# Kernel optimization log

Hardware: AMD Instinct MI355X
Metric: run time of the kernel (lower is better)

The kernel has to match this reference:

```python
import jax, jax.numpy as jnp
import numpy as np

B, S, E, H = 2, 2048, 2048, 16
HD = E // H  # head_dim = 128


def setup_inputs() -> dict:
    key = jax.random.key(0)
    ks = jax.random.split(key, 7)
    inp = {
        "query": jax.random.normal(ks[0], (B, S, E), dtype=jnp.float32),
        "key": jax.random.normal(ks[1], (B, S, E), dtype=jnp.float32),
        "value": jax.random.normal(ks[2], (B, S, E), dtype=jnp.float32),
        # qkv: Linear(E, 3E) -> weight [3E, E], bias [3E]
        "Wqkv": jax.random.normal(ks[3], (3 * E, E), dtype=jnp.float32) * (E ** -0.5),
        "bqkv": jnp.zeros((3 * E,), dtype=jnp.float32),
        # proj: Linear(E, E) (source bug-fixed; see notes)
        "Wproj": jax.random.normal(ks[4], (E, E), dtype=jnp.float32) * (E ** -0.5),
        "bproj": jnp.zeros((E,), dtype=jnp.float32),
    }
    return inp


def reference(query, key, value, Wqkv, bqkv, Wproj, bproj):
    # NB: `key` and `value` are unused by the original forward.
    b, s, _ = query.shape
    qkv = query @ Wqkv.T + bqkv                      # [B, S, 3E]
    qkv = qkv.reshape(b, s, H, 3 * HD).transpose(0, 2, 1, 3)  # [B, H, S, 3*HD]
    q = qkv[..., :HD]
    k = qkv[..., HD:2 * HD]
    v = qkv[..., 2 * HD:]
    # Source divides by scale_factor = HD**-0.5, i.e. MULTIPLIES by sqrt(HD).
    scores = jnp.einsum("bhqd,bhkd->bhqk", q, k) * (HD ** 0.5)
    attn = jax.nn.softmax(scores, axis=-1)           # dropout p=0 -> identity
    out = jnp.einsum("bhqk,bhkd->bhqd", attn, v)     # [B, H, S, HD]
    out = out.transpose(0, 2, 1, 3).reshape(b, s, E)  # [B, S, E]
    return out @ Wproj.T + bproj
```

## Files before the change

### kernel.cpp

```cpp
#include <hip/hip_runtime.h>

#define B_  2
#define S_  2048
#define E_  2048
#define H_  16
#define HD_ 128
#define M_  (B_*S_)
#define N1_ (3*E_)
#define K_  E_

typedef _Float16 f16;
typedef __attribute__((ext_vector_type(8))) _Float16 f16x8;
typedef __attribute__((ext_vector_type(4))) _Float16 f16x4;
typedef __attribute__((ext_vector_type(4))) float    f32x4;
typedef __attribute__((ext_vector_type(4))) float    fv4;

__device__ __forceinline__ void async16(const f16* g, f16* l) {
    __builtin_amdgcn_global_load_lds(
        (const __attribute__((address_space(1))) unsigned int*)g,
        (__attribute__((address_space(3))) unsigned int*)l, 16, 0, 0);
}

__device__ __forceinline__ int swz8(int row, int g) {
    return row * 64 + ((g ^ (row & 7)) << 3);
}
__device__ __forceinline__ int swz16(int row, int g) {
    return row * 128 + ((g ^ (row & 15)) << 3);
}

__device__ __forceinline__ void stage_swz8(const f16* __restrict__ src, int ldg,
                                           f16* lds, int w, int lane) {
#pragma unroll
    for (int i = 0; i < 4; ++i) {
        int p = (w * 4 + i) * 64 + lane;
        int row = p >> 3, gl = p & 7;
        int gs = gl ^ (row & 7);
        async16(src + (size_t)row * ldg + gs * 8, lds + (size_t)p * 8);
    }
}

__device__ __forceinline__ void stage_swz16(const f16* __restrict__ src, int ldg,
                                            f16* lds, int w, int lane) {
#pragma unroll
    for (int i = 0; i < 8; ++i) {
        int p = (w * 8 + i) * 64 + lane;
        int row = p >> 4, gl = p & 15;
        int gs = gl ^ (row & 15);
        async16(src + (size_t)row * ldg + gs * 8, lds + (size_t)p * 8);
    }
}

__device__ __forceinline__ void split8(fv4 a0, fv4 a1, float scale, f16x8& hi, f16x8& lo) {
    float x[8] = {a0.x, a0.y, a0.z, a0.w, a1.x, a1.y, a1.z, a1.w};
#pragma unroll
    for (int e = 0; e < 8; ++e) {
        float xs = x[e] * scale;
        f16 h = (f16)xs;
        hi[e] = h;
        lo[e] = (f16)(xs - (float)h);
    }
}

__global__ void split_f32(const float* __restrict__ src, f16* __restrict__ hi,
                          f16* __restrict__ lo, float scale, int n8) {
    int i = blockIdx.x * blockDim.x + threadIdx.x;
    if (i < n8) {
        fv4 a0 = ((const fv4*)src)[2 * i];
        fv4 a1 = ((const fv4*)src)[2 * i + 1];
        f16x8 h, l;
        split8(a0, a1, scale, h, l);
        ((f16x8*)hi)[i] = h;
        ((f16x8*)lo)[i] = l;
    }
}

__global__ void cvt_f32_f16(const float* __restrict__ src, f16* __restrict__ dst, int n4) {
    int i = blockIdx.x * blockDim.x + threadIdx.x;
    if (i < n4) {
        fv4 v = ((const fv4*)src)[i];
        f16x4 h;
        h.x = (f16)v.x; h.y = (f16)v.y; h.z = (f16)v.z; h.w = (f16)v.w;
        ((f16x4*)dst)[i] = h;
    }
}

template <bool AsyncA>
__global__ __launch_bounds__(256) void gemm_qkv(
    const float* __restrict__ A, const f16* __restrict__ A_hi, const f16* __restrict__ A_lo,
    const f16* __restrict__ W_hi, const f16* __restrict__ W_lo, const float* __restrict__ bias,
    f16* __restrict__ qh, f16* __restrict__ kh, f16* __restrict__ vT)
{
    __shared__ f16 As_hi[128 * 64];
    __shared__ f16 As_lo[128 * 64];
    __shared__ f16 Bs_hi[128 * 64];
    __shared__ f16 Bs_lo[128 * 64];
    const int t = threadIdx.x;
    const int w = t >> 6, lane = t & 63, quad = lane >> 4, l15 = lane & 15;
    const int m0 = blockIdx.y * 128, n0 = blockIdx.x * 128;
    const int wm = (w & 1) * 64, wn = (w >> 1) * 64;
    const int tile_part = (n0 % 384) >> 7;
    const bool need_lo = (tile_part != 2);

    f32x4 acc[4][4];
#pragma unroll
    for (int i = 0; i < 4; ++i)
#pragma unroll
        for (int j = 0; j < 4; ++j) { acc[i][j].x = 0.f; acc[i][j].y = 0.f; acc[i][j].z = 0.f; acc[i][j].w = 0.f; }

    for (int kb = 0; kb < K_ / 64; ++kb) {
        stage_swz8(W_hi + (size_t)n0 * K_ + kb * 64, K_, Bs_hi, w, lane);
        if (need_lo)
            stage_swz8(W_lo + (size_t)n0 * K_ + kb * 64, K_, Bs_lo, w, lane);
        if (AsyncA) {
            stage_swz8(A_hi + (size_t)m0 * K_ + kb * 64, K_, As_hi, w, lane);
            if (need_lo)
                stage_swz8(A_lo + (size_t)m0 * K_ + kb * 64, K_, As_lo, w, lane);
        } else {
            const float* Ag = A + (size_t)m0 * K_ + kb * 64;
#pragma unroll
            for (int i = 0; i < 4; ++i) {
                int gid = t + i * 256;
                int row = gid >> 3, g = gid & 7;
                const float* ap = Ag + (size_t)row * K_ + g * 8;
                fv4 a0 = *(const fv4*)ap;
                fv4 a1 = *(const fv4*)(ap + 4);
                f16x8 hi, lo;
                split8(a0, a1, 1.0f, hi, lo);
                *(f16x8*)&As_hi[swz8(row, g)] = hi;
                *(f16x8*)&As_lo[swz8(row, g)] = lo;
            }
        }
        __syncthreads();

#pragma unroll
        for (int ks = 0; ks < 2; ++ks) {
            f16x8 ah[4], al[4], bh[4], bl[4];
            int g = ks * 4 + quad;
#pragma unroll
            for (int mt = 0; mt < 4; ++mt) {
                int row = wm + mt * 16 + l15;
                ah[mt] = *(const f16x8*)&As_hi[swz8(row, g)];
                al[mt] = *(const f16x8*)&As_lo[swz8(row, g)];
            }
#pragma unroll
            for (int nt = 0; nt < 4; ++nt) {
                int row = wn + nt * 16 + l15;
                bh[nt] = *(const f16x8*)&Bs_hi[swz8(row, g)];
                bl[nt] = *(const f16x8*)&Bs_lo[swz8(row, g)];
            }
#pragma unroll
            for (int mt = 0; mt < 4; ++mt)
#pragma unroll
                for (int nt = 0; nt < 4; ++nt) {
                    acc[mt][nt] = __builtin_amdgcn_mfma_f32_16x16x32_f16(ah[mt], bh[nt], acc[mt][nt], 0, 0, 0);
                    if (need_lo) {
                        acc[mt][nt] = __builtin_amdgcn_mfma_f32_16x16x32_f16(ah[mt], bl[nt], acc[mt][nt], 0, 0, 0);
                        acc[mt][nt] = __builtin_amdgcn_mfma_f32_16x16x32_f16(al[mt], bh[nt], acc[mt][nt], 0, 0, 0);
                    }
                }
        }
        __syncthreads();
    }

    const float inv_s = 1.0f / 64.0f;
#pragma unroll
    for (int nt = 0; nt < 4; ++nt) {
        int n = n0 + wn + nt * 16 + l15;
        float bs = bias[n];
        int h = n / 384;
        int r = n % 384;
        int part = r >> 7;
        int d = r & 127;
#pragma unroll
        for (int mt = 0; mt < 4; ++mt) {
            int mbase = m0 + wm + mt * 16 + quad * 4;
            int b = mbase >> 11, s = mbase & 2047;
            int bh = b * H_ + h;
            if (part == 2) {
                f16x4 pv;
                pv.x = (f16)(acc[mt][nt].x * inv_s + bs);
                pv.y = (f16)(acc[mt][nt].y * inv_s + bs);
                pv.z = (f16)(acc[mt][nt].z * inv_s + bs);
                pv.w = (f16)(acc[mt][nt].w * inv_s + bs);
                *(f16x4*)&vT[((size_t)bh * 128 + d) * 2048 + s] = pv;
            } else {
                f16* dst = (part == 0) ? qh : kh;
                size_t base = (size_t)bh * 2048 * 128;
#pragma unroll
                for (int reg = 0; reg < 4; ++reg)
                    dst[base + (size_t)(s + reg) * 128 + d] = (f16)(acc[mt][nt][reg] * inv_s + bs);
            }
        }
    }
}

__global__ __launch_bounds__(256) void attn(
    const f16* __restrict__ qh, const f16* __restrict__ kh, const f16* __restrict__ vT,
    f16* __restrict__ ao)
{
    __shared__ f16 Ks[128 * 128];
    __shared__ f16 Vts[128 * 128];
    const int t = threadIdx.x;
    const int w = t >> 6, lane = t & 63, quad = lane >> 4, l15 = lane & 15;
    const int bh = blockIdx.y;
    const int q0 = blockIdx.x * 128;
    const f16* Q  = qh + (size_t)bh * 2048 * 128;
    const f16* Kp = kh + (size_t)bh * 2048 * 128;
    const f16* Vp = vT + (size_t)bh * 128 * 2048;

    const float C2 = (float)(11.313708498984761 * 1.4426950408889634);

    f16x8 qf[2][4];
#pragma unroll
    for (int mt = 0; mt < 2; ++mt)
#pragma unroll
        for (int ks = 0; ks < 4; ++ks) {
            int row = q0 + w * 32 + mt * 16 + l15;
            qf[mt][ks] = *(const f16x8*)&Q[(size_t)row * 128 + ks * 32 + quad * 8];
        }

    f32x4 o[2][8];
    float mrow[2][4], lrow[2][4];
#pragma unroll
    for (int mt = 0; mt < 2; ++mt) {
#pragma unroll
        for (int dt = 0; dt < 8; ++dt) { o[mt][dt].x = 0.f; o[mt][dt].y = 0.f; o[mt][dt].z = 0.f; o[mt][dt].w = 0.f; }
#pragma unroll
        for (int reg = 0; reg < 4; ++reg) { mrow[mt][reg] = -1e30f; lrow[mt][reg] = 0.f; }
    }

    for (int j = 0; j < 16; ++j) {
        __syncthreads();
        stage_swz16(Kp + (size_t)(j * 128) * 128, 128, Ks, w, lane);
        stage_swz16(Vp + j * 128, 2048, Vts, w, lane);
        __syncthreads();

        f32x4 sa[2][8];
#pragma unroll
        for (int mt = 0; mt < 2; ++mt)
#pragma unroll
            for (int nt = 0; nt < 8; ++nt) { sa[mt][nt].x = 0.f; sa[mt][nt].y = 0.f; sa[mt][nt].z = 0.f; sa[mt][nt].w = 0.f; }
#pragma unroll
        for (int ks = 0; ks < 4; ++ks) {
            int g = ks * 4 + quad;
            f16x8 bf[8];
#pragma unroll
            for (int nt = 0; nt < 8; ++nt) { int row = nt * 16 + l15; bf[nt] = *(const f16x8*)&Ks[swz16(row, g)]; }
#pragma unroll
            for (int mt = 0; mt < 2; ++mt)
#pragma unroll
                for (int nt = 0; nt < 8; ++nt)
                    sa[mt][nt] = __builtin_amdgcn_mfma_f32_16x16x32_f16(qf[mt][ks], bf[nt], sa[mt][nt], 0, 0, 0);
        }

        float mnew[2][4], alpha[2][4];
#pragma unroll
        for (int mt = 0; mt < 2; ++mt)
#pragma unroll
            for (int reg = 0; reg < 4; ++reg) {
                float mx = sa[mt][0][reg];
#pragma unroll
                for (int nt = 1; nt < 8; ++nt) mx = fmaxf(mx, sa[mt][nt][reg]);
                mx *= C2;
#pragma unroll
                for (int d = 1; d < 16; d <<= 1) mx = fmaxf(mx, __shfl_xor(mx, d));
                float mn = fmaxf(mrow[mt][reg], mx);
                mnew[mt][reg]  = mn;
                alpha[mt][reg] = exp2f(mrow[mt][reg] - mn);
                mrow[mt][reg]  = mn;
            }
#pragma unroll
        for (int mt = 0; mt < 2; ++mt)
#pragma unroll
            for (int reg = 0; reg < 4; ++reg) {
                float rs = 0.f;
#pragma unroll
                for (int nt = 0; nt < 8; ++nt) {
                    float p = exp2f(sa[mt][nt][reg] * C2 - mnew[mt][reg]);
                    sa[mt][nt][reg] = p;
                    rs += p;
                }
#pragma unroll
                for (int d = 1; d < 16; d <<= 1) rs += __shfl_xor(rs, d);
                lrow[mt][reg] = lrow[mt][reg] * alpha[mt][reg] + rs;
#pragma unroll
                for (int dt = 0; dt < 8; ++dt) o[mt][dt][reg] *= alpha[mt][reg];
            }

        __syncthreads();
#pragma unroll
        for (int mt = 0; mt < 2; ++mt)
#pragma unroll
            for (int nt = 0; nt < 8; ++nt) {
                int col = nt * 16 + l15;
#pragma unroll
                for (int reg = 0; reg < 4; ++reg) {
                    int row = w * 32 + mt * 16 + quad * 4 + reg;
                    Ks[row * 128 + (((col >> 3) ^ (row & 15)) << 3) + (col & 7)] = (f16)sa[mt][nt][reg];
                }
            }
        __syncthreads();

#pragma unroll
        for (int ks = 0; ks < 4; ++ks) {
            int g = ks * 4 + quad;
            f16x8 pf[2], vf[8];
#pragma unroll
            for (int mt = 0; mt < 2; ++mt) { int row = w * 32 + mt * 16 + l15; pf[mt] = *(const f16x8*)&Ks[swz16(row, g)]; }
#pragma unroll
            for (int dt = 0; dt < 8; ++dt) { int row = dt * 16 + l15; vf[dt] = *(const f16x8*)&Vts[swz16(row, g)]; }
#pragma unroll
            for (int mt = 0; mt < 2; ++mt)
#pragma unroll
                for (int dt = 0; dt < 8; ++dt)
                    o[mt][dt] = __builtin_amdgcn_mfma_f32_16x16x32_f16(pf[mt], vf[dt], o[mt][dt], 0, 0, 0);
        }
    }

    const int b = bh >> 4, h = bh & 15;
#pragma unroll
    for (int mt = 0; mt < 2; ++mt) {
        float inv[4];
#pragma unroll
        for (int reg = 0; reg < 4; ++reg) inv[reg] = 1.0f / lrow[mt][reg];
#pragma unroll
        for (int dt = 0; dt < 8; ++dt) {
            int col = h * 128 + dt * 16 + l15;
#pragma unroll
            for (int reg = 0; reg < 4; ++reg) {
                int srow = q0 + w * 32 + mt * 16 + quad * 4 + reg;
                ao[(size_t)((b << 11) + srow) * 2048 + col] = (f16)(o[mt][dt][reg] * inv[reg]);
            }
        }
    }
}

__global__ __launch_bounds__(256) void gemm_proj(
    const f16* __restrict__ A, const f16* __restrict__ W, const float* __restrict__ bias,
    float* __restrict__ out)
{
    __shared__ f16 As[128 * 64];
    __shared__ f16 Bs[128 * 64];
    const int t = threadIdx.x;
    const int w = t >> 6, lane = t & 63, quad = lane >> 4, l15 = lane & 15;
    const int m0 = blockIdx.y * 128, n0 = blockIdx.x * 128;
    const int wm = (w & 1) * 64, wn = (w >> 1) * 64;

    f32x4 acc[4][4];
#pragma unroll
    for (int i = 0; i < 4; ++i)
#pragma unroll
        for (int j = 0; j < 4; ++j) { acc[i][j].x = 0.f; acc[i][j].y = 0.f; acc[i][j].z = 0.f; acc[i][j].w = 0.f; }

    for (int kb = 0; kb < K_ / 64; ++kb) {
        stage_swz8(A + (size_t)m0 * K_ + kb * 64, K_, As, w, lane);
        stage_swz8(W + (size_t)n0 * K_ + kb * 64, K_, Bs, w, lane);
        __syncthreads();
#pragma unroll
        for (int ks = 0; ks < 2; ++ks) {
            f16x8 af[4], bf[4];
            int g = ks * 4 + quad;
#pragma unroll
            for (int mt = 0; mt < 4; ++mt) { int row = wm + mt * 16 + l15; af[mt] = *(const f16x8*)&As[swz8(row, g)]; }
#pragma unroll
            for (int nt = 0; nt < 4; ++nt) { int row = wn + nt * 16 + l15; bf[nt] = *(const f16x8*)&Bs[swz8(row, g)]; }
#pragma unroll
            for (int mt = 0; mt < 4; ++mt)
#pragma unroll
                for (int nt = 0; nt < 4; ++nt)
                    acc[mt][nt] = __builtin_amdgcn_mfma_f32_16x16x32_f16(af[mt], bf[nt], acc[mt][nt], 0, 0, 0);
        }
        __syncthreads();
    }

#pragma unroll
    for (int nt = 0; nt < 4; ++nt) {
        int n = n0 + wn + nt * 16 + l15;
        float bs = bias[n];
#pragma unroll
        for (int mt = 0; mt < 4; ++mt) {
            int mbase = m0 + wm + mt * 16 + quad * 4;
#pragma unroll
            for (int reg = 0; reg < 4; ++reg)
                out[(size_t)(mbase + reg) * 2048 + n] = acc[mt][nt][reg] + bs;
        }
    }
}

extern "C" void kernel_launch(void* const* d_in, const int* in_sizes, int n_in,
                              void* d_out, int out_size, void* d_ws, size_t ws_size,
                              hipStream_t stream) {
    const float* query = (const float*)d_in[0];
    const float* Wqkv  = (const float*)d_in[3];
    const float* bqkv  = (const float*)d_in[4];
    const float* Wproj = (const float*)d_in[5];
    const float* bproj = (const float*)d_in[6];
    float* out = (float*)d_out;

    char* ws = (char*)d_ws;
    const size_t MB = 1024ull * 1024ull;
    const bool big = (ws_size >= 128 * MB);

    f16 *A_hi, *A_lo, *W_hi, *W_lo, *qh, *kh, *vT, *ao, *w2;
    if (big) {
        A_hi = (f16*)(ws);
        A_lo = (f16*)(ws + 16 * MB);
        W_hi = (f16*)(ws + 32 * MB);
        W_lo = (f16*)(ws + 56 * MB);
        qh   = (f16*)(ws + 80 * MB);
        kh   = (f16*)(ws + 96 * MB);
        vT   = (f16*)(ws + 112 * MB);
        ao   = (f16*)(ws);
        w2   = (f16*)(ws + 56 * MB);
    } else {
        if (ws_size < 96 * MB) return;
        A_hi = A_lo = nullptr;
        W_hi = (f16*)(ws);
        W_lo = (f16*)(ws + 24 * MB);
        qh   = (f16*)(ws + 48 * MB);
        kh   = (f16*)(ws + 64 * MB);
        vT   = (f16*)(ws + 80 * MB);
        ao   = (f16*)(ws);
        w2   = (f16*)(ws + 24 * MB);
    }

    if (big)
        split_f32<<<(M_ * K_ / 8 + 255) / 256, 256, 0, stream>>>(query, A_hi, A_lo, 1.0f, M_ * K_ / 8);
    split_f32<<<(N1_ * K_ / 8 + 255) / 256, 256, 0, stream>>>(Wqkv, W_hi, W_lo, 64.0f, N1_ * K_ / 8);

    if (big)
        gemm_qkv<true><<<dim3(N1_ / 128, M_ / 128), 256, 0, stream>>>(query, A_hi, A_lo, W_hi, W_lo, bqkv, qh, kh, vT);
    else
        gemm_qkv<false><<<dim3(N1_ / 128, M_ / 128), 256, 0, stream>>>(query, A_hi, A_lo, W_hi, W_lo, bqkv, qh, kh, vT);

    cvt_f32_f16<<<(E_ * E_ / 4 + 255) / 256, 256, 0, stream>>>(Wproj, w2, E_ * E_ / 4);

    attn<<<dim3(S_ / 128, B_ * H_), 256, 0, stream>>>(qh, kh, vT, ao);
    gemm_proj<<<dim3(E_ / 128, M_ / 128), 256, 0, stream>>>(ao, w2, bproj, out);
}
```

Before: 639.5 us.

## Double-buffer 64-key K/V tiles in attention and use private P scratch

The attention kernel now processes 64-key tiles instead of 128 and double-buffers K and V in LDS. The next tile's async loads are issued right after the single top-of-loop barrier, so they overlap with the current tile's QK^T, softmax and PV work. P now goes to a separate per-wave LDS region (Ps) rather than overwriting the K tile, which removes two of the three barriers per iteration. In exchange, LDS use grows from 64KB to 80KB and there are twice as many online-softmax rescale steps, since each tile is smaller.

```diff
diff --git a/kernel.cpp b/kernel.cpp
--- a/kernel.cpp
+++ b/kernel.cpp
@@ -39,14 +39,22 @@
     }
 }
 
-__device__ __forceinline__ void stage_swz16(const f16* __restrict__ src, int ldg,
-                                            f16* lds, int w, int lane) {
-#pragma unroll
-    for (int i = 0; i < 8; ++i) {
-        int p = (w * 8 + i) * 64 + lane;
+__device__ __forceinline__ void stage_k64(const f16* __restrict__ src, f16* lds, int t) {
+#pragma unroll
+    for (int i = 0; i < 4; ++i) {
+        int p = i * 256 + t;
         int row = p >> 4, gl = p & 15;
         int gs = gl ^ (row & 15);
-        async16(src + (size_t)row * ldg + gs * 8, lds + (size_t)p * 8);
+        async16(src + (size_t)row * 128 + gs * 8, lds + (size_t)p * 8);
+    }
+}
+__device__ __forceinline__ void stage_v64(const f16* __restrict__ src, f16* lds, int t) {
+#pragma unroll
+    for (int i = 0; i < 4; ++i) {
+        int p = i * 256 + t;
+        int row = p >> 3, gl = p & 7;
+        int gs = gl ^ (row & 7);
+        async16(src + (size_t)row * 2048 + gs * 8, lds + (size_t)p * 8);
     }
 }
 
@@ -198,8 +206,9 @@
     const f16* __restrict__ qh, const f16* __restrict__ kh, const f16* __restrict__ vT,
     f16* __restrict__ ao)
 {
-    __shared__ f16 Ks[128 * 128];
-    __shared__ f16 Vts[128 * 128];
+    __shared__ f16 Kb[2][64 * 128];
+    __shared__ f16 Vb[2][128 * 64];
+    __shared__ f16 Ps[128 * 64];
     const int t = threadIdx.x;
     const int w = t >> 6, lane = t & 63, quad = lane >> 4, l15 = lane & 15;
     const int bh = blockIdx.y;
@@ -229,27 +238,32 @@
         for (int reg = 0; reg < 4; ++reg) { mrow[mt][reg] = -1e30f; lrow[mt][reg] = 0.f; }
     }
 
-    for (int j = 0; j < 16; ++j) {
+    stage_k64(Kp, Kb[0], t);
+    stage_v64(Vp, Vb[0], t);
+
+    for (int j = 0; j < 32; ++j) {
         __syncthreads();
-        stage_swz16(Kp + (size_t)(j * 128) * 128, 128, Ks, w, lane);
-        stage_swz16(Vp + j * 128, 2048, Vts, w, lane);
-        __syncthreads();
-
-        f32x4 sa[2][8];
+        const int cur = j & 1;
+        if (j < 31) {
+            stage_k64(Kp + (size_t)(j + 1) * 64 * 128, Kb[cur ^ 1], t);
+            stage_v64(Vp + (j + 1) * 64, Vb[cur ^ 1], t);
+        }
+
+        f32x4 sa[2][4];
 #pragma unroll
         for (int mt = 0; mt < 2; ++mt)
 #pragma unroll
-            for (int nt = 0; nt < 8; ++nt) { sa[mt][nt].x = 0.f; sa[mt][nt].y = 0.f; sa[mt][nt].z = 0.f; sa[mt][nt].w = 0.f; }
+            for (int nt = 0; nt < 4; ++nt) { sa[mt][nt].x = 0.f; sa[mt][nt].y = 0.f; sa[mt][nt].z = 0.f; sa[mt][nt].w = 0.f; }
 #pragma unroll
         for (int ks = 0; ks < 4; ++ks) {
             int g = ks * 4 + quad;
-            f16x8 bf[8];
-#pragma unroll
-            for (int nt = 0; nt < 8; ++nt) { int row = nt * 16 + l15; bf[nt] = *(const f16x8*)&Ks[swz16(row, g)]; }
+            f16x8 bf[4];
+#pragma unroll
+            for (int nt = 0; nt < 4; ++nt) { int row = nt * 16 + l15; bf[nt] = *(const f16x8*)&Kb[cur][swz16(row, g)]; }
 #pragma unroll
             for (int mt = 0; mt < 2; ++mt)
 #pragma unroll
-                for (int nt = 0; nt < 8; ++nt)
+                for (int nt = 0; nt < 4; ++nt)
                     sa[mt][nt] = __builtin_amdgcn_mfma_f32_16x16x32_f16(qf[mt][ks], bf[nt], sa[mt][nt], 0, 0, 0);
         }
 
@@ -260,7 +274,7 @@
             for (int reg = 0; reg < 4; ++reg) {
                 float mx = sa[mt][0][reg];
 #pragma unroll
-                for (int nt = 1; nt < 8; ++nt) mx = fmaxf(mx, sa[mt][nt][reg]);
+                for (int nt = 1; nt < 4; ++nt) mx = fmaxf(mx, sa[mt][nt][reg]);
                 mx *= C2;
 #pragma unroll
                 for (int d = 1; d < 16; d <<= 1) mx = fmaxf(mx, __shfl_xor(mx, d));
@@ -275,7 +289,7 @@
             for (int reg = 0; reg < 4; ++reg) {
                 float rs = 0.f;
 #pragma unroll
-                for (int nt = 0; nt < 8; ++nt) {
+                for (int nt = 0; nt < 4; ++nt) {
                     float p = exp2f(sa[mt][nt][reg] * C2 - mnew[mt][reg]);
                     sa[mt][nt][reg] = p;
                     rs += p;
@@ -287,28 +301,26 @@
                 for (int dt = 0; dt < 8; ++dt) o[mt][dt][reg] *= alpha[mt][reg];
             }
 
-        __syncthreads();
 #pragma unroll
         for (int mt = 0; mt < 2; ++mt)
 #pragma unroll
-            for (int nt = 0; nt < 8; ++nt) {
+            for (int nt = 0; nt < 4; ++nt) {
                 int col = nt * 16 + l15;
 #pragma unroll
                 for (int reg = 0; reg < 4; ++reg) {
                     int row = w * 32 + mt * 16 + quad * 4 + reg;
-                    Ks[row * 128 + (((col >> 3) ^ (row & 15)) << 3) + (col & 7)] = (f16)sa[mt][nt][reg];
+                    Ps[row * 64 + (((col >> 3) ^ (row & 7)) << 3) + (col & 7)] = (f16)sa[mt][nt][reg];
                 }
             }
-        __syncthreads();
-
-#pragma unroll
-        for (int ks = 0; ks < 4; ++ks) {
+
+#pragma unroll
+        for (int ks = 0; ks < 2; ++ks) {
             int g = ks * 4 + quad;
             f16x8 pf[2], vf[8];
 #pragma unroll
-            for (int mt = 0; mt < 2; ++mt) { int row = w * 32 + mt * 16 + l15; pf[mt] = *(const f16x8*)&Ks[swz16(row, g)]; }
-#pragma unroll
-            for (int dt = 0; dt < 8; ++dt) { int row = dt * 16 + l15; vf[dt] = *(const f16x8*)&Vts[swz16(row, g)]; }
+            for (int mt = 0; mt < 2; ++mt) { int row = w * 32 + mt * 16 + l15; pf[mt] = *(const f16x8*)&Ps[swz8(row, g)]; }
+#pragma unroll
+            for (int dt = 0; dt < 8; ++dt) { int row = dt * 16 + l15; vf[dt] = *(const f16x8*)&Vb[cur][swz8(row, g)]; }
 #pragma unroll
             for (int mt = 0; mt < 2; ++mt)
 #pragma unroll
```

Result: slower. 707.1 us (+10.6%).
